# Optimization experiments

Measured on AMD Instinct MI355X. Metric: run time of the kernel, lower is better.

The kernel has to match this reference:

```python
import jax, jax.numpy as jnp
import numpy as np

N = 50000      # nodes
E = 800000     # edges (avg degree 16)
D_IN = 128
D_H = 256
NUM_LAYERS = 5


def setup_inputs() -> dict:
    key = jax.random.key(0)
    ks = jax.random.split(key, 12)
    s_in = 1.0 / np.sqrt(D_IN)
    s_h = 1.0 / np.sqrt(D_H)
    x = jax.random.normal(ks[0], (N, D_IN), jnp.float32)
    edge_index = jax.random.randint(ks[1], (2, E), 0, N, jnp.int32)
    eps_all = jnp.zeros((NUM_LAYERS,), jnp.float32)
    # torch Linear layout: weight [out, in], y = x @ W.T + b; scaled for stability
    w0_l0 = jax.random.normal(ks[2], (D_H, D_IN), jnp.float32) * s_in
    b0_l0 = jax.random.normal(ks[3], (D_H,), jnp.float32) * 0.01
    w1_l0 = jax.random.normal(ks[4], (D_H, D_H), jnp.float32) * s_h
    b1_l0 = jax.random.normal(ks[5], (D_H,), jnp.float32) * 0.01
    w0_rest = jax.random.normal(ks[6], (4, D_H, D_H), jnp.float32) * s_h
    b0_rest = jax.random.normal(ks[7], (4, D_H), jnp.float32) * 0.01
    w1_rest = jax.random.normal(ks[8], (4, D_H, D_H), jnp.float32) * s_h
    b1_rest = jax.random.normal(ks[9], (4, D_H), jnp.float32) * 0.01
    return {"x": x, "edge_index": edge_index, "eps_all": eps_all,
            "w0_l0": w0_l0, "b0_l0": b0_l0, "w1_l0": w1_l0, "b1_l0": b1_l0,
            "w0_rest": w0_rest, "b0_rest": b0_rest, "w1_rest": w1_rest, "b1_rest": b1_rest}


def _gin_layer(x, src, dst, eps, w0, b0, w1, b1):
    # gather source-node features along edges, scatter-sum into destination nodes
    aggr = jax.ops.segment_sum(x[src], dst, num_segments=N)  # [N, d]
    h = (1.0 + eps) * x + aggr
    h = jax.nn.relu(h @ w0.T + b0)   # dropout p=0.0 -> identity
    h = h @ w1.T + b1
    return jax.nn.relu(h)            # inter-layer ReLU from the trace


def reference(x, edge_index, eps_all, w0_l0, b0_l0, w1_l0, b1_l0,
              w0_rest, b0_rest, w1_rest, b1_rest):
    src = edge_index[0]  # edge_index_j (messages come from row 0)
    dst = edge_index[1]  # edge_index_i (aggregated at row 1)
    h = _gin_layer(x, src, dst, eps_all[0], w0_l0, b0_l0, w1_l0, b1_l0)
    for i in range(4):  # layers 1..4, identical shapes
        h = _gin_layer(h, src, dst, eps_all[i + 1],
                       w0_rest[i], b0_rest[i], w1_rest[i], b1_rest[i])
    return h  # [N, D_H]
```

## Files before the change

### kernel.cpp

```cpp
#include <hip/hip_runtime.h>
#include <hip/hip_bf16.h>
#include <stdint.h>

#define D_IN 128
#define D_H 256
#define NLAYERS 5

typedef __bf16 bf16x8 __attribute__((ext_vector_type(8)));
typedef __bf16 bf16x4 __attribute__((ext_vector_type(4)));
typedef float f32x4 __attribute__((ext_vector_type(4)));
typedef unsigned short u16x8 __attribute__((ext_vector_type(8)));

#define MID_STRIDE 260

__device__ inline __bf16 f2bf(float f) {
  __hip_bfloat16 h = __float2bfloat16(f);
  __bf16 r;
  __builtin_memcpy(&r, &h, sizeof(r));
  return r;
}

__device__ inline unsigned short bfbits(float f) {
  __hip_bfloat16 h = __float2bfloat16(f);
  unsigned short s;
  __builtin_memcpy(&s, &h, 2);
  return s;
}

__device__ inline float bf2f(unsigned short u) {
  return __uint_as_float((unsigned)u << 16);
}

__global__ void conv_weights(const float* __restrict__ a, const float* __restrict__ b,
                             const float* __restrict__ c, const float* __restrict__ d,
                             __hip_bfloat16* __restrict__ out) {
  int gid = blockIdx.x * blockDim.x + threadIdx.x;
  if (gid >= 622592) return;
  float v;
  if (gid < 32768) v = a[gid];
  else if (gid < 98304) v = b[gid - 32768];
  else if (gid < 360448) v = c[gid - 98304];
  else v = d[gid - 360448];
  out[gid] = __float2bfloat16(v);
}

__global__ void zero_ints(int* __restrict__ p, int n) {
  int i = blockIdx.x * blockDim.x + threadIdx.x;
  if (i < n) p[i] = 0;
}

__global__ void hist_kernel(const int* __restrict__ ei, int E, int* __restrict__ deg) {
  int e = blockIdx.x * blockDim.x + threadIdx.x;
  if (e < E) atomicAdd(&deg[ei[E + e]], 1);
}

__global__ __launch_bounds__(256) void block_sums(const int* __restrict__ deg,
                                                  int* __restrict__ bsum, int N) {
  int t = threadIdx.x;
  int idx = blockIdx.x * 1024 + t * 4;
  int4 v = {0, 0, 0, 0};
  if (idx + 3 < N) v = *reinterpret_cast<const int4*>(deg + idx);
  else {
    if (idx + 0 < N) v.x = deg[idx + 0];
    if (idx + 1 < N) v.y = deg[idx + 1];
    if (idx + 2 < N) v.z = deg[idx + 2];
    if (idx + 3 < N) v.w = deg[idx + 3];
  }
  int s = v.x + v.y + v.z + v.w;
#pragma unroll
  for (int off = 32; off > 0; off >>= 1) s += __shfl_down(s, off);
  __shared__ int ws[4];
  int lane = t & 63, w = t >> 6;
  if (lane == 0) ws[w] = s;
  __syncthreads();
  if (t == 0) bsum[blockIdx.x] = ws[0] + ws[1] + ws[2] + ws[3];
}

__global__ void scan_bsums(int* __restrict__ bsum, int nb) {
  int t = threadIdx.x;
  int orig = (t < nb) ? bsum[t] : 0;
  int v = orig;
#pragma unroll
  for (int off = 1; off < 64; off <<= 1) {
    int u = __shfl_up(v, off);
    if (t >= off) v += u;
  }
  if (t < nb) bsum[t] = v - orig;
}

__global__ __launch_bounds__(256) void scan_apply(const int* __restrict__ deg,
                                                  const int* __restrict__ bsum_ex,
                                                  int* __restrict__ row_start, int N) {
  int t = threadIdx.x;
  int idx = blockIdx.x * 1024 + t * 4;
  int4 v = {0, 0, 0, 0};
  if (idx + 3 < N) v = *reinterpret_cast<const int4*>(deg + idx);
  else {
    if (idx + 0 < N) v.x = deg[idx + 0];
    if (idx + 1 < N) v.y = deg[idx + 1];
    if (idx + 2 < N) v.z = deg[idx + 2];
    if (idx + 3 < N) v.w = deg[idx + 3];
  }
  int s = v.x + v.y + v.z + v.w;
  int lane = t & 63, w = t >> 6;
  int sc = s;
#pragma unroll
  for (int off = 1; off < 64; off <<= 1) {
    int u = __shfl_up(sc, off);
    if (lane >= off) sc += u;
  }
  __shared__ int woff[4];
  if (lane == 63) woff[w] = sc;
  __syncthreads();
  int boff = bsum_ex[blockIdx.x];
#pragma unroll
  for (int i = 0; i < 4; ++i)
    if (i < w) boff += woff[i];
  int ex = boff + sc - s;
  if (idx + 3 < N) {
    int4 o;
    o.x = ex;
    o.y = ex + v.x;
    o.z = ex + v.x + v.y;
    o.w = ex + v.x + v.y + v.z;
    *reinterpret_cast<int4*>(row_start + idx) = o;
  } else {
    if (idx + 0 < N) row_start[idx + 0] = ex;
    if (idx + 1 < N) row_start[idx + 1] = ex + v.x;
    if (idx + 2 < N) row_start[idx + 2] = ex + v.x + v.y;
    if (idx + 3 < N) row_start[idx + 3] = ex + v.x + v.y + v.z;
  }
}

__global__ void fill_kernel(const int* __restrict__ ei, int E,
                            const int* __restrict__ row_start,
                            int* __restrict__ cursor, int* __restrict__ csr) {
  int e = blockIdx.x * blockDim.x + threadIdx.x;
  if (e >= E) return;
  int d = ei[E + e];
  int p = atomicAdd(&cursor[d], 1);
  csr[row_start[d] + p] = ei[e];
}

template <int D, bool IN_F32>
__global__ __launch_bounds__(256) void aggregate(const void* __restrict__ hin,
                                                 const int* __restrict__ csr,
                                                 const int* __restrict__ row_start,
                                                 const int* __restrict__ deg,
                                                 const float* __restrict__ eps_all,
                                                 int layer,
                                                 unsigned short* __restrict__ pre,
                                                 int N) {
  const int half = threadIdx.x >> 5;
  const int lane = threadIdx.x & 31;
  const int node = blockIdx.x * 8 + half;
  if (node >= N) return;

  const int start = row_start[node];
  const int cnt = deg[node];

  if (IN_F32) {
    const float* hf = (const float*)hin;
    f32x4 self = *reinterpret_cast<const f32x4*>(hf + (size_t)node * D + lane * 4);
    f32x4 acc = 0.0f;
    for (int base = 0; base < cnt; base += 32) {
      int m = cnt - base;
      if (m > 32) m = 32;
      int idx = (lane < m) ? csr[start + base + lane] : 0;
      int i = 0;
      for (; i + 4 <= m; i += 4) {
        int s0 = __shfl(idx, i + 0, 32);
        int s1 = __shfl(idx, i + 1, 32);
        int s2 = __shfl(idx, i + 2, 32);
        int s3 = __shfl(idx, i + 3, 32);
        f32x4 v0 = *reinterpret_cast<const f32x4*>(hf + (size_t)s0 * D + lane * 4);
        f32x4 v1 = *reinterpret_cast<const f32x4*>(hf + (size_t)s1 * D + lane * 4);
        f32x4 v2 = *reinterpret_cast<const f32x4*>(hf + (size_t)s2 * D + lane * 4);
        f32x4 v3 = *reinterpret_cast<const f32x4*>(hf + (size_t)s3 * D + lane * 4);
        acc += (v0 + v1) + (v2 + v3);
      }
      for (; i < m; ++i) {
        int s0 = __shfl(idx, i, 32);
        acc += *reinterpret_cast<const f32x4*>(hf + (size_t)s0 * D + lane * 4);
      }
    }
    float epsv = 1.0f + eps_all[layer];
    acc += self * epsv;
    ushort4 o;
    o.x = bfbits(acc[0]);
    o.y = bfbits(acc[1]);
    o.z = bfbits(acc[2]);
    o.w = bfbits(acc[3]);
    *reinterpret_cast<ushort4*>(pre + (size_t)node * D + lane * 4) = o;
  } else {
    const unsigned short* hb = (const unsigned short*)hin;
    u16x8 su = *reinterpret_cast<const u16x8*>(hb + (size_t)node * D + lane * 8);
    float acc[8];
#pragma unroll
    for (int j = 0; j < 8; ++j) acc[j] = 0.0f;
    for (int base = 0; base < cnt; base += 32) {
      int m = cnt - base;
      if (m > 32) m = 32;
      int idx = (lane < m) ? csr[start + base + lane] : 0;
      int i = 0;
      for (; i + 4 <= m; i += 4) {
        int s0 = __shfl(idx, i + 0, 32);
        int s1 = __shfl(idx, i + 1, 32);
        int s2 = __shfl(idx, i + 2, 32);
        int s3 = __shfl(idx, i + 3, 32);
        u16x8 u0 = *reinterpret_cast<const u16x8*>(hb + (size_t)s0 * D + lane * 8);
        u16x8 u1 = *reinterpret_cast<const u16x8*>(hb + (size_t)s1 * D + lane * 8);
        u16x8 u2 = *reinterpret_cast<const u16x8*>(hb + (size_t)s2 * D + lane * 8);
        u16x8 u3 = *reinterpret_cast<const u16x8*>(hb + (size_t)s3 * D + lane * 8);
#pragma unroll
        for (int j = 0; j < 8; ++j)
          acc[j] += (bf2f(u0[j]) + bf2f(u1[j])) + (bf2f(u2[j]) + bf2f(u3[j]));
      }
      for (; i < m; ++i) {
        int s0 = __shfl(idx, i, 32);
        u16x8 u0 = *reinterpret_cast<const u16x8*>(hb + (size_t)s0 * D + lane * 8);
#pragma unroll
        for (int j = 0; j < 8; ++j) acc[j] += bf2f(u0[j]);
      }
    }
    float epsv = 1.0f + eps_all[layer];
    u16x8 o;
#pragma unroll
    for (int j = 0; j < 8; ++j) o[j] = bfbits(acc[j] + epsv * bf2f(su[j]));
    *reinterpret_cast<u16x8*>(pre + (size_t)node * D + lane * 8) = o;
  }
}

template <int K0, bool OUT_BF16>
__global__ __launch_bounds__(256) void gin_mlp(const __hip_bfloat16* __restrict__ Ap,
                                               const __hip_bfloat16* __restrict__ W0,
                                               const float* __restrict__ b0,
                                               const __hip_bfloat16* __restrict__ W1,
                                               const float* __restrict__ b1,
                                               void* __restrict__ Outp, int Nrows) {
  __shared__ unsigned short Abuf[64 * MID_STRIDE];

  const int row0 = blockIdx.x * 64;

  {
    constexpr int CPR = K0 / 8;
    constexpr int TOT = 64 * CPR;
    const unsigned short* As = (const unsigned short*)Ap;
#pragma unroll
    for (int c = threadIdx.x; c < TOT; c += 256) {
      int row = c / CPR;
      int col = (c % CPR) * 8;
      int grow = row0 + row;
      if (grow > Nrows - 1) grow = Nrows - 1;
      u16x8 v = *reinterpret_cast<const u16x8*>(As + (size_t)grow * K0 + col);
      *reinterpret_cast<u16x8*>(Abuf + row * MID_STRIDE + col) = v;
    }
  }
  __syncthreads();

  const int lane = threadIdx.x & 63;
  const int wave = threadIdx.x >> 6;
  const int l15 = lane & 15;
  const int kg = lane >> 4;
  const int col0 = wave * 64;

  const __hip_bfloat16* w0row[4];
#pragma unroll
  for (int ct = 0; ct < 4; ++ct)
    w0row[ct] = W0 + (size_t)(col0 + ct * 16 + l15) * K0 + kg * 8;

  f32x4 acc0[2][2][4];
#pragma unroll
  for (int t = 0; t < 2; ++t)
#pragma unroll
    for (int rt = 0; rt < 2; ++rt)
#pragma unroll
      for (int ct = 0; ct < 4; ++ct) acc0[t][rt][ct] = 0.0f;

#pragma unroll
  for (int kk = 0; kk < K0 / 32; ++kk) {
    const int off = kk * 32;
    bf16x8 bfr[4];
#pragma unroll
    for (int ct = 0; ct < 4; ++ct)
      bfr[ct] = *reinterpret_cast<const bf16x8*>(w0row[ct] + off);
    bf16x8 afr[2][2];
#pragma unroll
    for (int t = 0; t < 2; ++t)
#pragma unroll
      for (int rt = 0; rt < 2; ++rt) {
        const unsigned short* p =
            Abuf + (t * 32 + rt * 16 + l15) * MID_STRIDE + off + kg * 8;
        bf16x4 lo = *reinterpret_cast<const bf16x4*>(p);
        bf16x4 hi = *reinterpret_cast<const bf16x4*>(p + 4);
        bf16x8 a;
#pragma unroll
        for (int j = 0; j < 4; ++j) {
          a[j] = lo[j];
          a[j + 4] = hi[j];
        }
        afr[t][rt] = a;
      }
#pragma unroll
    for (int t = 0; t < 2; ++t)
#pragma unroll
      for (int rt = 0; rt < 2; ++rt)
#pragma unroll
        for (int ct = 0; ct < 4; ++ct)
          acc0[t][rt][ct] = __builtin_amdgcn_mfma_f32_16x16x32_bf16(
              afr[t][rt], bfr[ct], acc0[t][rt][ct], 0, 0, 0);
  }
  __syncthreads();

#pragma unroll
  for (int t = 0; t < 2; ++t)
#pragma unroll
    for (int ct = 0; ct < 4; ++ct) {
      int col = col0 + ct * 16 + l15;
      float bv = b0[col];
#pragma unroll
      for (int rt = 0; rt < 2; ++rt)
#pragma unroll
        for (int i = 0; i < 4; ++i) {
          int row_l = t * 32 + rt * 16 + kg * 4 + i;
          Abuf[row_l * MID_STRIDE + col] =
              bfbits(fmaxf(acc0[t][rt][ct][i] + bv, 0.0f));
        }
    }
  __syncthreads();

  const unsigned short* w1row[4];
#pragma unroll
  for (int ct = 0; ct < 4; ++ct)
    w1row[ct] =
        (const unsigned short*)W1 + (size_t)(col0 + ct * 16 + l15) * D_H + kg * 8;

  f32x4 acc1[2][2][4];
#pragma unroll
  for (int t = 0; t < 2; ++t)
#pragma unroll
    for (int rt = 0; rt < 2; ++rt)
#pragma unroll
      for (int ct = 0; ct < 4; ++ct) acc1[t][rt][ct] = 0.0f;

#pragma unroll
  for (int kk = 0; kk < D_H / 32; ++kk) {
    const int off = kk * 32;
    bf16x8 wfr[4];
#pragma unroll
    for (int ct = 0; ct < 4; ++ct)
      wfr[ct] = *reinterpret_cast<const bf16x8*>(w1row[ct] + off);
    bf16x8 afr[2][2];
#pragma unroll
    for (int t = 0; t < 2; ++t)
#pragma unroll
      for (int rt = 0; rt < 2; ++rt) {
        const unsigned short* p =
            Abuf + (t * 32 + rt * 16 + l15) * MID_STRIDE + off + kg * 8;
        bf16x4 lo = *reinterpret_cast<const bf16x4*>(p);
        bf16x4 hi = *reinterpret_cast<const bf16x4*>(p + 4);
        bf16x8 a;
#pragma unroll
        for (int j = 0; j < 4; ++j) {
          a[j] = lo[j];
          a[j + 4] = hi[j];
        }
        afr[t][rt] = a;
      }
#pragma unroll
    for (int t = 0; t < 2; ++t)
#pragma unroll
      for (int rt = 0; rt < 2; ++rt)
#pragma unroll
        for (int ct = 0; ct < 4; ++ct)
          acc1[t][rt][ct] = __builtin_amdgcn_mfma_f32_16x16x32_bf16(
              afr[t][rt], wfr[ct], acc1[t][rt][ct], 0, 0, 0);
  }

#pragma unroll
  for (int t = 0; t < 2; ++t)
#pragma unroll
    for (int ct = 0; ct < 4; ++ct) {
      int col = col0 + ct * 16 + l15;
      float bv = b1[col];
#pragma unroll
      for (int rt = 0; rt < 2; ++rt)
#pragma unroll
        for (int i = 0; i < 4; ++i) {
          int row = row0 + t * 32 + rt * 16 + kg * 4 + i;
          if (row < Nrows) {
            float v = fmaxf(acc1[t][rt][ct][i] + bv, 0.0f);
            if (OUT_BF16)
              ((__hip_bfloat16*)Outp)[(size_t)row * D_H + col] = __float2bfloat16(v);
            else
              ((float*)Outp)[(size_t)row * D_H + col] = v;
          }
        }
    }
}

extern "C" void kernel_launch(void* const* d_in, const int* in_sizes, int n_in,
                              void* d_out, int out_size, void* d_ws, size_t ws_size,
                              hipStream_t stream) {
  const float* x = (const float*)d_in[0];
  const int* ei = (const int*)d_in[1];
  const float* eps_all = (const float*)d_in[2];
  const float* w0_l0 = (const float*)d_in[3];
  const float* b0_l0 = (const float*)d_in[4];
  const float* w1_l0 = (const float*)d_in[5];
  const float* b1_l0 = (const float*)d_in[6];
  const float* w0_rest = (const float*)d_in[7];
  const float* b0_rest = (const float*)d_in[8];
  const float* w1_rest = (const float*)d_in[9];
  const float* b1_rest = (const float*)d_in[10];

  const int N = in_sizes[0] / D_IN;
  const int E = in_sizes[1] / 2;

  char* ws = (char*)d_ws;
  const size_t node_bf = (size_t)N * D_H * sizeof(unsigned short);
  unsigned short* h = (unsigned short*)ws;
  unsigned short* pre = (unsigned short*)(ws + node_bf);
  char* p = ws + 2 * node_bf;
  __hip_bfloat16* wbf = (__hip_bfloat16*)p;
  p += 622592 * sizeof(__hip_bfloat16);
  int* deg = (int*)p;
  int* cursor = deg + N;
  int* row_start = cursor + N;
  int* bsum = row_start + N;
  int* csr = bsum + 64;

  __hip_bfloat16* w0_l0_bf = wbf;
  __hip_bfloat16* w1_l0_bf = wbf + 32768;
  __hip_bfloat16* w0_rest_bf = wbf + 98304;
  __hip_bfloat16* w1_rest_bf = w0_rest_bf + 262144;

  conv_weights<<<(622592 + 255) / 256, 256, 0, stream>>>(w0_l0, w1_l0, w0_rest,
                                                         w1_rest, wbf);

  const int nb = (N + 1023) / 1024;
  zero_ints<<<(2 * N + 255) / 256, 256, 0, stream>>>(deg, 2 * N);
  hist_kernel<<<(E + 255) / 256, 256, 0, stream>>>(ei, E, deg);
  block_sums<<<nb, 256, 0, stream>>>(deg, bsum, N);
  scan_bsums<<<1, 64, 0, stream>>>(bsum, nb);
  scan_apply<<<nb, 256, 0, stream>>>(deg, bsum, row_start, N);
  fill_kernel<<<(E + 255) / 256, 256, 0, stream>>>(ei, E, row_start, cursor, csr);

  const int gemmBlocks = (N + 63) / 64;
  const int aggBlocks = (N + 7) / 8;

  for (int layer = 0; layer < NLAYERS; ++layer) {
    const __hip_bfloat16* w0 =
        (layer == 0) ? w0_l0_bf : w0_rest_bf + (size_t)(layer - 1) * 65536;
    const float* b0 = (layer == 0) ? b0_l0 : b0_rest + (size_t)(layer - 1) * 256;
    const __hip_bfloat16* w1 =
        (layer == 0) ? w1_l0_bf : w1_rest_bf + (size_t)(layer - 1) * 65536;
    const float* b1 = (layer == 0) ? b1_l0 : b1_rest + (size_t)(layer - 1) * 256;

    if (layer == 0) {
      aggregate<D_IN, true><<<aggBlocks, 256, 0, stream>>>(
          x, csr, row_start, deg, eps_all, layer, pre, N);
      gin_mlp<D_IN, true><<<gemmBlocks, 256, 0, stream>>>(
          (const __hip_bfloat16*)pre, w0, b0, w1, b1, h, N);
    } else {
      aggregate<D_H, false><<<aggBlocks, 256, 0, stream>>>(
          h, csr, row_start, deg, eps_all, layer, pre, N);
      if (layer == NLAYERS - 1)
        gin_mlp<D_H, false><<<gemmBlocks, 256, 0, stream>>>(
            (const __hip_bfloat16*)pre, w0, b0, w1, b1, d_out, N);
      else
        gin_mlp<D_H, true><<<gemmBlocks, 256, 0, stream>>>(
            (const __hip_bfloat16*)pre, w0, b0, w1, b1, h, N);
    }
  }
}
```

Before: 626.6 us.

## Gather layer-0 features in bf16, unroll gathers by 8, halve MLP row tile

Converts x to bf16 up front, folded into the weight-conversion kernel, so the first aggregation gathers half as many bytes per edge. The aggregation inner loop now issues 8 independent row loads before accumulating, using packed bf16 unpack helpers, to raise memory-level parallelism. The fused MLP kernel processes 32 rows per block instead of 64, which doubles the block count and cuts register and LDS use per block. The trade-offs are an extra conversion pass over x, rounding of layer-0 inputs to bf16, and more reloads of the weights from global memory.

```diff
diff --git a/kernel.cpp b/kernel.cpp
--- a/kernel.cpp
+++ b/kernel.cpp
@@ -12,13 +12,6 @@
 typedef unsigned short u16x8 __attribute__((ext_vector_type(8)));
 
 #define MID_STRIDE 260
-
-__device__ inline __bf16 f2bf(float f) {
-  __hip_bfloat16 h = __float2bfloat16(f);
-  __bf16 r;
-  __builtin_memcpy(&r, &h, sizeof(r));
-  return r;
-}
 
 __device__ inline unsigned short bfbits(float f) {
   __hip_bfloat16 h = __float2bfloat16(f);
@@ -27,21 +20,38 @@
   return s;
 }
 
-__device__ inline float bf2f(unsigned short u) {
-  return __uint_as_float((unsigned)u << 16);
-}
-
-__global__ void conv_weights(const float* __restrict__ a, const float* __restrict__ b,
-                             const float* __restrict__ c, const float* __restrict__ d,
-                             __hip_bfloat16* __restrict__ out) {
+__device__ inline unsigned packbf(float lo, float hi) {
+  return (unsigned)bfbits(lo) | ((unsigned)bfbits(hi) << 16);
+}
+
+__device__ inline void addbf2(float& a, float& b, unsigned u) {
+  a += __uint_as_float(u << 16);
+  b += __uint_as_float(u & 0xffff0000u);
+}
+
+__device__ inline void addbf2s(float& a, float& b, unsigned u, float s) {
+  a += s * __uint_as_float(u << 16);
+  b += s * __uint_as_float(u & 0xffff0000u);
+}
+
+__global__ void conv_inputs(const float* __restrict__ x, const float* __restrict__ a,
+                            const float* __restrict__ b, const float* __restrict__ c,
+                            const float* __restrict__ d,
+                            __hip_bfloat16* __restrict__ xb,
+                            __hip_bfloat16* __restrict__ wb, int nx) {
   int gid = blockIdx.x * blockDim.x + threadIdx.x;
+  if (gid < nx) {
+    xb[gid] = __float2bfloat16(x[gid]);
+    return;
+  }
+  gid -= nx;
   if (gid >= 622592) return;
   float v;
   if (gid < 32768) v = a[gid];
   else if (gid < 98304) v = b[gid - 32768];
   else if (gid < 360448) v = c[gid - 98304];
   else v = d[gid - 360448];
-  out[gid] = __float2bfloat16(v);
+  wb[gid] = __float2bfloat16(v);
 }
 
 __global__ void zero_ints(int* __restrict__ p, int n) {
@@ -142,8 +152,8 @@
   csr[row_start[d] + p] = ei[e];
 }
 
-template <int D, bool IN_F32>
-__global__ __launch_bounds__(256) void aggregate(const void* __restrict__ hin,
+template <int D>
+__global__ __launch_bounds__(256) void aggregate(const unsigned short* __restrict__ hb,
                                                  const int* __restrict__ csr,
                                                  const int* __restrict__ row_start,
                                                  const int* __restrict__ deg,
@@ -151,6 +161,7 @@
                                                  int layer,
                                                  unsigned short* __restrict__ pre,
                                                  int N) {
+  constexpr int PL = D / 32;
   const int half = threadIdx.x >> 5;
   const int lane = threadIdx.x & 31;
   const int node = blockIdx.x * 8 + half;
@@ -158,76 +169,115 @@
 
   const int start = row_start[node];
   const int cnt = deg[node];
-
-  if (IN_F32) {
-    const float* hf = (const float*)hin;
-    f32x4 self = *reinterpret_cast<const f32x4*>(hf + (size_t)node * D + lane * 4);
-    f32x4 acc = 0.0f;
+  const float epsv = 1.0f + eps_all[layer];
+
+  float acc[PL];
+#pragma unroll
+  for (int j = 0; j < PL; ++j) acc[j] = 0.0f;
+
+  if (D == 256) {
+    const uint4* base_p = (const uint4*)hb;
+    uint4 su = *reinterpret_cast<const uint4*>(hb + (size_t)node * D + lane * 8);
     for (int base = 0; base < cnt; base += 32) {
       int m = cnt - base;
       if (m > 32) m = 32;
       int idx = (lane < m) ? csr[start + base + lane] : 0;
       int i = 0;
+      for (; i + 8 <= m; i += 8) {
+        uint4 q[8];
+#pragma unroll
+        for (int r = 0; r < 8; ++r) {
+          int s = __shfl(idx, i + r, 32);
+          q[r] = *reinterpret_cast<const uint4*>(hb + (size_t)s * D + lane * 8);
+        }
+#pragma unroll
+        for (int r = 0; r < 8; ++r) {
+          addbf2(acc[0], acc[1], q[r].x);
+          addbf2(acc[2], acc[3], q[r].y);
+          addbf2(acc[4], acc[5], q[r].z);
+          addbf2(acc[6], acc[7], q[r].w);
+        }
+      }
       for (; i + 4 <= m; i += 4) {
-        int s0 = __shfl(idx, i + 0, 32);
-        int s1 = __shfl(idx, i + 1, 32);
-        int s2 = __shfl(idx, i + 2, 32);
-        int s3 = __shfl(idx, i + 3, 32);
-        f32x4 v0 = *reinterpret_cast<const f32x4*>(hf + (size_t)s0 * D + lane * 4);
-        f32x4 v1 = *reinterpret_cast<const f32x4*>(hf + (size_t)s1 * D + lane * 4);
-        f32x4 v2 = *reinterpret_cast<const f32x4*>(hf + (size_t)s2 * D + lane * 4);
-        f32x4 v3 = *reinterpret_cast<const f32x4*>(hf + (size_t)s3 * D + lane * 4);
-        acc += (v0 + v1) + (v2 + v3);
+        uint4 q[4];
+#pragma unroll
+        for (int r = 0; r < 4; ++r) {
+          int s = __shfl(idx, i + r, 32);
+          q[r] = *reinterpret_cast<const uint4*>(hb + (size_t)s * D + lane * 8);
+        }
+#pragma unroll
+        for (int r = 0; r < 4; ++r) {
+          addbf2(acc[0], acc[1], q[r].x);
+          addbf2(acc[2], acc[3], q[r].y);
+          addbf2(acc[4], acc[5], q[r].z);
+          addbf2(acc[6], acc[7], q[r].w);
+        }
       }
       for (; i < m; ++i) {
-        int s0 = __shfl(idx, i, 32);
-        acc += *reinterpret_cast<const f32x4*>(hf + (size_t)s0 * D + lane * 4);
+        int s = __shfl(idx, i, 32);
+        uint4 q = *reinterpret_cast<const uint4*>(hb + (size_t)s * D + lane * 8);
+        addbf2(acc[0], acc[1], q.x);
+        addbf2(acc[2], acc[3], q.y);
+        addbf2(acc[4], acc[5], q.z);
+        addbf2(acc[6], acc[7], q.w);
       }
     }
-    float epsv = 1.0f + eps_all[layer];
-    acc += self * epsv;
-    ushort4 o;
-    o.x = bfbits(acc[0]);
-    o.y = bfbits(acc[1]);
-    o.z = bfbits(acc[2]);
-    o.w = bfbits(acc[3]);
-    *reinterpret_cast<ushort4*>(pre + (size_t)node * D + lane * 4) = o;
+    addbf2s(acc[0], acc[1], su.x, epsv);
+    addbf2s(acc[2], acc[3], su.y, epsv);
+    addbf2s(acc[4], acc[5], su.z, epsv);
+    addbf2s(acc[6], acc[7], su.w, epsv);
+    uint4 o;
+    o.x = packbf(acc[0], acc[1]);
+    o.y = packbf(acc[2], acc[3]);
+    o.z = packbf(acc[4], acc[5]);
+    o.w = packbf(acc[6], acc[7]);
+    *reinterpret_cast<uint4*>(pre + (size_t)node * D + lane * 8) = o;
   } else {
-    const unsigned short* hb = (const unsigned short*)hin;
-    u16x8 su = *reinterpret_cast<const u16x8*>(hb + (size_t)node * D + lane * 8);
-    float acc[8];
-#pragma unroll
-    for (int j = 0; j < 8; ++j) acc[j] = 0.0f;
+    uint2 su = *reinterpret_cast<const uint2*>(hb + (size_t)node * D + lane * 4);
     for (int base = 0; base < cnt; base += 32) {
       int m = cnt - base;
       if (m > 32) m = 32;
       int idx = (lane < m) ? csr[start + base + lane] : 0;
       int i = 0;
+      for (; i + 8 <= m; i += 8) {
+        uint2 q[8];
+#pragma unroll
+        for (int r = 0; r < 8; ++r) {
+          int s = __shfl(idx, i + r, 32);
+          q[r] = *reinterpret_cast<const uint2*>(hb + (size_t)s * D + lane * 4);
+        }
+#pragma unroll
+        for (int r = 0; r < 8; ++r) {
+          addbf2(acc[0], acc[1], q[r].x);
+          addbf2(acc[2], acc[3], q[r].y);
+        }
+      }
       for (; i + 4 <= m; i += 4) {
-        int s0 = __shfl(idx, i + 0, 32);
-        int s1 = __shfl(idx, i + 1, 32);
-        int s2 = __shfl(idx, i + 2, 32);
-        int s3 = __shfl(idx, i + 3, 32);
-        u16x8 u0 = *reinterpret_cast<const u16x8*>(hb + (size_t)s0 * D + lane * 8);
-        u16x8 u1 = *reinterpret_cast<const u16x8*>(hb + (size_t)s1 * D + lane * 8);
-        u16x8 u2 = *reinterpret_cast<const u16x8*>(hb + (size_t)s2 * D + lane * 8);
-        u16x8 u3 = *reinterpret_cast<const u16x8*>(hb + (size_t)s3 * D + lane * 8);
-#pragma unroll
-        for (int j = 0; j < 8; ++j)
-          acc[j] += (bf2f(u0[j]) + bf2f(u1[j])) + (bf2f(u2[j]) + bf2f(u3[j]));
+        uint2 q[4];
+#pragma unroll
+        for (int r = 0; r < 4; ++r) {
+          int s = __shfl(idx, i + r, 32);
+          q[r] = *reinterpret_cast<const uint2*>(hb + (size_t)s * D + lane * 4);
+        }
+#pragma unroll
+        for (int r = 0; r < 4; ++r) {
+          addbf2(acc[0], acc[1], q[r].x);
+          addbf2(acc[2], acc[3], q[r].y);
+        }
       }
       for (; i < m; ++i) {
-        int s0 = __shfl(idx, i, 32);
-        u16x8 u0 = *reinterpret_cast<const u16x8*>(hb + (size_t)s0 * D + lane * 8);
-#pragma unroll
-        for (int j = 0; j < 8; ++j) acc[j] += bf2f(u0[j]);
+        int s = __shfl(idx, i, 32);
+        uint2 q = *reinterpret_cast<const uint2*>(hb + (size_t)s * D + lane * 4);
+        addbf2(acc[0], acc[1], q.x);
+        addbf2(acc[2], acc[3], q.y);
       }
     }
-    float epsv = 1.0f + eps_all[layer];
-    u16x8 o;
-#pragma unroll
-    for (int j = 0; j < 8; ++j) o[j] = bfbits(acc[j] + epsv * bf2f(su[j]));
-    *reinterpret_cast<u16x8*>(pre + (size_t)node * D + lane * 8) = o;
+    addbf2s(acc[0], acc[1], su.x, epsv);
+    addbf2s(acc[2], acc[3], su.y, epsv);
+    uint2 o;
+    o.x = packbf(acc[0], acc[1]);
+    o.y = packbf(acc[2], acc[3]);
+    *reinterpret_cast<uint2*>(pre + (size_t)node * D + lane * 4) = o;
   }
 }
 
@@ -238,13 +288,13 @@
                                                const __hip_bfloat16* __restrict__ W1,
                                                const float* __restrict__ b1,
                                                void* __restrict__ Outp, int Nrows) {
-  __shared__ unsigned short Abuf[64 * MID_STRIDE];
-
-  const int row0 = blockIdx.x * 64;
+  __shared__ unsigned short Abuf[32 * MID_STRIDE];
+
+  const int row0 = blockIdx.x * 32;
 
   {
     constexpr int CPR = K0 / 8;
-    constexpr int TOT = 64 * CPR;
+    constexpr int TOT = 32 * CPR;
     const unsigned short* As = (const unsigned short*)Ap;
 #pragma unroll
     for (int c = threadIdx.x; c < TOT; c += 256) {
@@ -269,13 +319,11 @@
   for (int ct = 0; ct < 4; ++ct)
     w0row[ct] = W0 + (size_t)(col0 + ct * 16 + l15) * K0 + kg * 8;
 
-  f32x4 acc0[2][2][4];
-#pragma unroll
-  for (int t = 0; t < 2; ++t)
-#pragma unroll
-    for (int rt = 0; rt < 2; ++rt)
-#pragma unroll
-      for (int ct = 0; ct < 4; ++ct) acc0[t][rt][ct] = 0.0f;
+  f32x4 acc0[2][4];
+#pragma unroll
+  for (int rt = 0; rt < 2; ++rt)
+#pragma unroll
+    for (int ct = 0; ct < 4; ++ct) acc0[rt][ct] = 0.0f;
 
 #pragma unroll
   for (int kk = 0; kk < K0 / 32; ++kk) {
@@ -284,49 +332,41 @@
 #pragma unroll
     for (int ct = 0; ct < 4; ++ct)
       bfr[ct] = *reinterpret_cast<const bf16x8*>(w0row[ct] + off);
-    bf16x8 afr[2][2];
-#pragma unroll
-    for (int t = 0; t < 2; ++t)
-#pragma unroll
-      for (int rt = 0; rt < 2; ++rt) {
-        const unsigned short* p =
-            Abuf + (t * 32 + rt * 16 + l15) * MID_STRIDE + off + kg * 8;
-        bf16x4 lo = *reinterpret_cast<const bf16x4*>(p);
-        bf16x4 hi = *reinterpret_cast<const bf16x4*>(p + 4);
-        bf16x8 a;
-#pragma unroll
-        for (int j = 0; j < 4; ++j) {
-          a[j] = lo[j];
-          a[j + 4] = hi[j];
-        }
-        afr[t][rt] = a;
-      }
-#pragma unroll
-    for (int t = 0; t < 2; ++t)
-#pragma unroll
-      for (int rt = 0; rt < 2; ++rt)
-#pragma unroll
-        for (int ct = 0; ct < 4; ++ct)
-          acc0[t][rt][ct] = __builtin_amdgcn_mfma_f32_16x16x32_bf16(
-              afr[t][rt], bfr[ct], acc0[t][rt][ct], 0, 0, 0);
+    bf16x8 afr[2];
+#pragma unroll
+    for (int rt = 0; rt < 2; ++rt) {
+      const unsigned short* p = Abuf + (rt * 16 + l15) * MID_STRIDE + off + kg * 8;
+      bf16x4 lo = *reinterpret_cast<const bf16x4*>(p);
+      bf16x4 hi = *reinterpret_cast<const bf16x4*>(p + 4);
+      bf16x8 a;
+#pragma unroll
+      for (int j = 0; j < 4; ++j) {
+        a[j] = lo[j];
+        a[j + 4] = hi[j];
+      }
+      afr[rt] = a;
+    }
+#pragma unroll
+    for (int rt = 0; rt < 2; ++rt)
+#pragma unroll
+      for (int ct = 0; ct < 4; ++ct)
+        acc0[rt][ct] = __builtin_amdgcn_mfma_f32_16x16x32_bf16(afr[rt], bfr[ct],
+                                                               acc0[rt][ct], 0, 0, 0);
   }
   __syncthreads();
 
 #pragma unroll
-  for (int t = 0; t < 2; ++t)
-#pragma unroll
-    for (int ct = 0; ct < 4; ++ct) {
-      int col = col0 + ct * 16 + l15;
-      float bv = b0[col];
-#pragma unroll
-      for (int rt = 0; rt < 2; ++rt)
-#pragma unroll
-        for (int i = 0; i < 4; ++i) {
-          int row_l = t * 32 + rt * 16 + kg * 4 + i;
-          Abuf[row_l * MID_STRIDE + col] =
-              bfbits(fmaxf(acc0[t][rt][ct][i] + bv, 0.0f));
-        }
-    }
+  for (int ct = 0; ct < 4; ++ct) {
+    int col = col0 + ct * 16 + l15;
+    float bv = b0[col];
+#pragma unroll
+    for (int rt = 0; rt < 2; ++rt)
+#pragma unroll
+      for (int i = 0; i < 4; ++i) {
+        int row_l = rt * 16 + kg * 4 + i;
+        Abuf[row_l * MID_STRIDE + col] = bfbits(fmaxf(acc0[rt][ct][i] + bv, 0.0f));
+      }
+  }
   __syncthreads();
 
   const unsigned short* w1row[4];
@@ -335,13 +375,11 @@
     w1row[ct] =
         (const unsigned short*)W1 + (size_t)(col0 + ct * 16 + l15) * D_H + kg * 8;
 
-  f32x4 acc1[2][2][4];
-#pragma unroll
-  for (int t = 0; t < 2; ++t)
-#pragma unroll
-    for (int rt = 0; rt < 2; ++rt)
-#pragma unroll
-      for (int ct = 0; ct < 4; ++ct) acc1[t][rt][ct] = 0.0f;
+  f32x4 acc1[2][4];
+#pragma unroll
+  for (int rt = 0; rt < 2; ++rt)
+#pragma unroll
+    for (int ct = 0; ct < 4; ++ct) acc1[rt][ct] = 0.0f;
 
 #pragma unroll
   for (int kk = 0; kk < D_H / 32; ++kk) {
@@ -350,53 +388,46 @@
 #pragma unroll
     for (int ct = 0; ct < 4; ++ct)
       wfr[ct] = *reinterpret_cast<const bf16x8*>(w1row[ct] + off);
-    bf16x8 afr[2][2];
-#pragma unroll
-    for (int t = 0; t < 2; ++t)
-#pragma unroll
-      for (int rt = 0; rt < 2; ++rt) {
-        const unsigned short* p =
-            Abuf + (t * 32 + rt * 16 + l15) * MID_STRIDE + off + kg * 8;
-        bf16x4 lo = *reinterpret_cast<const bf16x4*>(p);
-        bf16x4 hi = *reinterpret_cast<const bf16x4*>(p + 4);
-        bf16x8 a;
-#pragma unroll
-        for (int j = 0; j < 4; ++j) {
-          a[j] = lo[j];
-          a[j + 4] = hi[j];
-        }
-        afr[t][rt] = a;
-      }
-#pragma unroll
-    for (int t = 0; t < 2; ++t)
-#pragma unroll
-      for (int rt = 0; rt < 2; ++rt)
-#pragma unroll
-        for (int ct = 0; ct < 4; ++ct)
-          acc1[t][rt][ct] = __builtin_amdgcn_mfma_f32_16x16x32_bf16(
-              afr[t][rt], wfr[ct], acc1[t][rt][ct], 0, 0, 0);
-  }
-
-#pragma unroll
-  for (int t = 0; t < 2; ++t)
-#pragma unroll
-    for (int ct = 0; ct < 4; ++ct) {
-      int col = col0 + ct * 16 + l15;
-      float bv = b1[col];
-#pragma unroll
-      for (int rt = 0; rt < 2; ++rt)
-#pragma unroll
-        for (int i = 0; i < 4; ++i) {
-          int row = row0 + t * 32 + rt * 16 + kg * 4 + i;
-          if (row < Nrows) {
-            float v = fmaxf(acc1[t][rt][ct][i] + bv, 0.0f);
-            if (OUT_BF16)
-              ((__hip_bfloat16*)Outp)[(size_t)row * D_H + col] = __float2bfloat16(v);
-            else
-              ((float*)Outp)[(size_t)row * D_H + col] = v;
-          }
-        }
+    bf16x8 afr[2];
+#pragma unroll
+    for (int rt = 0; rt < 2; ++rt) {
+      const unsigned short* p = Abuf + (rt * 16 + l15) * MID_STRIDE + off + kg * 8;
+      bf16x4 lo = *reinterpret_cast<const bf16x4*>(p);
+      bf16x4 hi = *reinterpret_cast<const bf16x4*>(p + 4);
+      bf16x8 a;
+#pragma unroll
+      for (int j = 0; j < 4; ++j) {
+        a[j] = lo[j];
+        a[j + 4] = hi[j];
+      }
+      afr[rt] = a;
     }
+#pragma unroll
+    for (int rt = 0; rt < 2; ++rt)
+#pragma unroll
+      for (int ct = 0; ct < 4; ++ct)
+        acc1[rt][ct] = __builtin_amdgcn_mfma_f32_16x16x32_bf16(afr[rt], wfr[ct],
+                                                               acc1[rt][ct], 0, 0, 0);
+  }
+
+#pragma unroll
+  for (int ct = 0; ct < 4; ++ct) {
+    int col = col0 + ct * 16 + l15;
+    float bv = b1[col];
+#pragma unroll
+    for (int rt = 0; rt < 2; ++rt)
+#pragma unroll
+      for (int i = 0; i < 4; ++i) {
+        int row = row0 + rt * 16 + kg * 4 + i;
+        if (row < Nrows) {
+          float v = fmaxf(acc1[rt][ct][i] + bv, 0.0f);
+          if (OUT_BF16)
+            ((__hip_bfloat16*)Outp)[(size_t)row * D_H + col] = __float2bfloat16(v);
+          else
+            ((float*)Outp)[(size_t)row * D_H + col] = v;
+        }
+      }
+  }
 }
 
 extern "C" void kernel_launch(void* const* d_in, const int* in_sizes, int n_in,
@@ -416,12 +447,14 @@
 
   const int N = in_sizes[0] / D_IN;
   const int E = in_sizes[1] / 2;
+  const int NX = N * D_IN;
 
   char* ws = (char*)d_ws;
   const size_t node_bf = (size_t)N * D_H * sizeof(unsigned short);
   unsigned short* h = (unsigned short*)ws;
   unsigned short* pre = (unsigned short*)(ws + node_bf);
-  char* p = ws + 2 * node_bf;
+  unsigned short* xb = (unsigned short*)(ws + 2 * node_bf);
+  char* p = ws + 2 * node_bf + (size_t)NX * sizeof(unsigned short);
   __hip_bfloat16* wbf = (__hip_bfloat16*)p;
   p += 622592 * sizeof(__hip_bfloat16);
   int* deg = (int*)p;
@@ -435,8 +468,8 @@
   __hip_bfloat16* w0_rest_bf = wbf + 98304;
   __hip_bfloat16* w1_rest_bf = w0_rest_bf + 262144;
 
-  conv_weights<<<(622592 + 255) / 256, 256, 0, stream>>>(w0_l0, w1_l0, w0_rest,
-                                                         w1_rest, wbf);
+  conv_inputs<<<(NX + 622592 + 255) / 256, 256, 0, stream>>>(
+      x, w0_l0, w1_l0, w0_rest, w1_rest, (__hip_bfloat16*)xb, wbf, NX);
 
   const int nb = (N + 1023) / 1024;
   zero_ints<<<(2 * N + 255) / 256, 256, 0, stream>>>(deg, 2 * N);
@@ -446,7 +479,7 @@
   scan_apply<<<nb, 256, 0, stream>>>(deg, bsum, row_start, N);
   fill_kernel<<<(E + 255) / 256, 256, 0, stream>>>(ei, E, row_start, cursor, csr);
 
-  const int gemmBlocks = (N + 63) / 64;
+  const int gemmBlocks = (N + 31) / 32;
   const int aggBlocks = (N + 7) / 8;
 
   for (int layer = 0; layer < NLAYERS; ++layer) {
@@ -458,13 +491,13 @@
     const float* b1 = (layer == 0) ? b1_l0 : b1_rest + (size_t)(layer - 1) * 256;
 
     if (layer == 0) {
-      aggregate<D_IN, true><<<aggBlocks, 256, 0, stream>>>(
-          x, csr, row_start, deg, eps_all, layer, pre, N);
+      aggregate<D_IN><<<aggBlocks, 256, 0, stream>>>(xb, csr, row_start, deg,
+                                                     eps_all, layer, pre, N);
       gin_mlp<D_IN, true><<<gemmBlocks, 256, 0, stream>>>(
           (const __hip_bfloat16*)pre, w0, b0, w1, b1, h, N);
     } else {
-      aggregate<D_H, false><<<aggBlocks, 256, 0, stream>>>(
-          h, csr, row_start, deg, eps_all, layer, pre, N);
+      aggregate<D_H><<<aggBlocks, 256, 0, stream>>>(h, csr, row_start, deg,
+                                                    eps_all, layer, pre, N);
       if (layer == NLAYERS - 1)
         gin_mlp<D_H, false><<<gemmBlocks, 256, 0, stream>>>(
             (const __hip_bfloat16*)pre, w0, b0, w1, b1, d_out, N);
```

New measurement: 664.2 us. 6.0% more time.
